# Kernel tuning notes

Hardware: AMD Instinct MI355X
Metric: run time of the kernel (lower is better)

Reference implementation:

```python
import jax, jax.numpy as jnp
import numpy as np

D_IN = 1024
D_OUT = 1024
N = 4096


def setup_inputs() -> dict:
    key = jax.random.key(0)
    ks = jax.random.split(key, 7)
    s_in = 1.0 / np.sqrt(D_IN)
    return {
        "x": jax.random.normal(ks[0], (N, D_IN), dtype=jnp.float32),
        "W_q": jax.random.uniform(ks[1], (D_IN, D_OUT), jnp.float32, -s_in, s_in),
        "b_q": jax.random.uniform(ks[2], (D_OUT,), jnp.float32, -s_in, s_in),
        "W_k": jax.random.uniform(ks[3], (D_IN, D_OUT), jnp.float32, -s_in, s_in),
        "b_k": jax.random.uniform(ks[4], (D_OUT,), jnp.float32, -s_in, s_in),
        "W_v": jax.random.uniform(ks[5], (D_IN, D_OUT), jnp.float32, -s_in, s_in),
        "b_v": jax.random.uniform(ks[6], (D_OUT,), jnp.float32, -s_in, s_in),
    }


def reference(x, W_q, b_q, W_k, b_k, W_v, b_v):
    # QKV projections (Linear with bias): [N, d_out]
    q = x @ W_q + b_q
    k = x @ W_k + b_k
    v = x @ W_v + b_v
    # Full attention: scores [N, N], scaled by sqrt(d_out)
    scores = (q @ k.T) / jnp.sqrt(jnp.asarray(k.shape[-1], q.dtype))
    attn = jax.nn.softmax(scores, axis=-1)
    return attn @ v  # [N, d_out]
```

## Files before the change

### kernel.cpp

```cpp
#include <hip/hip_runtime.h>

typedef __attribute__((ext_vector_type(8))) short short8;
typedef __attribute__((ext_vector_type(4))) float f32x4;
typedef __attribute__((ext_vector_type(8))) unsigned short ushort8;

typedef const unsigned int __attribute__((address_space(1)))* gas1_t;
typedef unsigned int __attribute__((address_space(3)))* las3_t;

__device__ __forceinline__ void gload_lds16(const void* g, void* l) {
  __builtin_amdgcn_global_load_lds((gas1_t)g, (las3_t)l, 16, 0, 0);
}

__device__ __forceinline__ unsigned short f2bf(float f) {
  unsigned int u = __float_as_uint(f);
  u += 0x7FFFu + ((u >> 16) & 1u);
  return (unsigned short)(u >> 16);
}
__device__ __forceinline__ float bf2f(unsigned short b) {
  return __uint_as_float(((unsigned int)b) << 16);
}

__global__ __launch_bounds__(256) void conv_f32_bf16(const float* __restrict__ in,
                                                     unsigned short* __restrict__ out, int n8) {
  int i = blockIdx.x * 256 + threadIdx.x;
  if (i >= n8) return;
  const f32x4* p = (const f32x4*)(in + (size_t)i * 8);
  f32x4 a = p[0], b = p[1];
  ushort8 o;
  o[0]=f2bf(a[0]); o[1]=f2bf(a[1]); o[2]=f2bf(a[2]); o[3]=f2bf(a[3]);
  o[4]=f2bf(b[0]); o[5]=f2bf(b[1]); o[6]=f2bf(b[2]); o[7]=f2bf(b[3]);
  *(ushort8*)(out + (size_t)i * 8) = o;
}

__global__ __launch_bounds__(256) void transconv_w(const float* __restrict__ Wq,
                                                   const float* __restrict__ Wk,
                                                   const float* __restrict__ Wv,
                                                   unsigned short* __restrict__ out) {
  __shared__ unsigned short tile[64][66];
  const float* W = (blockIdx.z == 0) ? Wq : ((blockIdx.z == 1) ? Wk : Wv);
  unsigned short* O = out + (size_t)blockIdx.z * 1048576;
  const int bi = blockIdx.x * 64;
  const int bo = blockIdx.y * 64;
#pragma unroll
  for (int p = 0; p < 16; ++p) {
    int idx = p * 256 + threadIdx.x;
    int r = idx >> 6, c = idx & 63;
    tile[r][c] = f2bf(W[(size_t)(bi + r) * 1024 + bo + c]);
  }
  __syncthreads();
#pragma unroll
  for (int p = 0; p < 16; ++p) {
    int idx = p * 256 + threadIdx.x;
    int r = idx >> 6, c = idx & 63;
    O[(size_t)(bo + r) * 1024 + bi + c] = tile[c][r];
  }
}

__global__ __launch_bounds__(256) void trans_bf16(const unsigned short* __restrict__ in,
                                                  unsigned short* __restrict__ out, int R, int C) {
  __shared__ unsigned short tile[64][66];
  const int br = blockIdx.x * 64, bc = blockIdx.y * 64;
#pragma unroll
  for (int p = 0; p < 16; ++p) {
    int idx = p * 256 + threadIdx.x;
    int r = idx >> 6, c = idx & 63;
    tile[r][c] = in[(size_t)(br + r) * C + bc + c];
  }
  __syncthreads();
#pragma unroll
  for (int p = 0; p < 16; ++p) {
    int idx = p * 256 + threadIdx.x;
    int r = idx >> 6, c = idx & 63;
    out[(size_t)(bc + r) * R + br + c] = tile[c][r];
  }
}

__global__ __launch_bounds__(256) void reduce_pv(const unsigned short* __restrict__ P,
                                                 const float* __restrict__ rsum,
                                                 float* __restrict__ out) {
  int i = blockIdx.x * 256 + threadIdx.x;
  const int m = (i * 8) >> 10;
  const float inv = 1.0f / rsum[m];
  float s[8] = {0.f, 0.f, 0.f, 0.f, 0.f, 0.f, 0.f, 0.f};
#pragma unroll
  for (int z = 0; z < 4; ++z) {
    ushort8 v = *(const ushort8*)(P + (size_t)z * 4194304 + (size_t)i * 8);
#pragma unroll
    for (int j = 0; j < 8; ++j) s[j] += bf2f(v[j]);
  }
  f32x4 o0, o1;
#pragma unroll
  for (int j = 0; j < 4; ++j) { o0[j] = s[j] * inv; o1[j] = s[4 + j] * inv; }
  f32x4* po = (f32x4*)(out + (size_t)i * 8);
  po[0] = o0; po[1] = o1;
}

template <int EPI>
__global__ __launch_bounds__(512, 1) void gemm256(
    const unsigned short* __restrict__ A, const unsigned short* __restrict__ B,
    int lda, int ldb, int K, void* __restrict__ C, int ldc,
    size_t strideBz, size_t strideCz,
    const float* __restrict__ bq, const float* __restrict__ bk, const float* __restrict__ bv,
    float scale, float* __restrict__ rsum) {
  __shared__ unsigned short As[2][2][8192];
  __shared__ unsigned short Bs[2][2][8192];
  const int tid = threadIdx.x;
  const int lane = tid & 63;
  const int w = tid >> 6;
  const int wr = w >> 2;
  const int wc = w & 3;
  const int l16 = lane & 15;
  const int q = lane >> 4;
  const int swq = (q ^ ((l16 >> 1) & 3)) * 8;

  const int nwgx = gridDim.x;
  const int nwg = nwgx * gridDim.y;
  const int lin = blockIdx.y * nwgx + blockIdx.x;
  const int swz = (lin & 7) * (nwg >> 3) + (lin >> 3);
  const int m0 = (swz / nwgx) * 256;
  const int n0 = (swz % nwgx) * 256;
  const int z = blockIdx.z;
  const unsigned short* Bz = B + (size_t)z * strideBz;
  const size_t koff = (EPI == 2) ? (size_t)z * K : 0;

  f32x4 acc[8][4];
#pragma unroll
  for (int i = 0; i < 8; ++i)
#pragma unroll
    for (int j = 0; j < 4; ++j) acc[i][j] = f32x4{0.f, 0.f, 0.f, 0.f};

  const unsigned short* apA[2][2];
  const unsigned short* apB[2][2];
#pragma unroll
  for (int ks = 0; ks < 2; ++ks)
#pragma unroll
    for (int j = 0; j < 2; ++j) {
      const int g = (j << 9) + tid;
      const int row = g >> 2;
      const int sq = (g & 3) ^ ((row >> 1) & 3);
      apA[ks][j] = A + (size_t)(m0 + row) * lda + koff + ks * 32 + sq * 8;
      apB[ks][j] = Bz + (size_t)(n0 + row) * ldb + koff + ks * 32 + sq * 8;
    }

#define STG_A(BUF, KS, K0)                                      \
  do {                                                          \
    gload_lds16(apA[KS][0] + (K0), &As[BUF][KS][tid * 8]);      \
    gload_lds16(apA[KS][1] + (K0), &As[BUF][KS][(512 + tid) * 8]); \
  } while (0)
#define STG_B(BUF, KS, K0)                                      \
  do {                                                          \
    gload_lds16(apB[KS][0] + (K0), &Bs[BUF][KS][tid * 8]);      \
    gload_lds16(apB[KS][1] + (K0), &Bs[BUF][KS][(512 + tid) * 8]); \
  } while (0)

  short8 bfr[4], afr[4];
#define LDB4(KS, BUF)                                                         \
  do {                                                                        \
    _Pragma("unroll") for (int _n = 0; _n < 4; ++_n) {                        \
      const int _r = wc * 64 + _n * 16 + l16;                                 \
      bfr[_n] = *(const short8*)(&Bs[BUF][KS][_r * 32 + swq]);                \
    }                                                                         \
  } while (0)
#define LDA4(KS, MH, BUF)                                                     \
  do {                                                                        \
    _Pragma("unroll") for (int _m = 0; _m < 4; ++_m) {                        \
      const int _r = wr * 128 + ((MH) * 4 + _m) * 16 + l16;                   \
      afr[_m] = *(const short8*)(&As[BUF][KS][_r * 32 + swq]);                \
    }                                                                         \
  } while (0)
#define MMP(MH)                                                               \
  do {                                                                        \
    __builtin_amdgcn_s_setprio(1);                                            \
    _Pragma("unroll") for (int _m = 0; _m < 4; ++_m)                          \
      _Pragma("unroll") for (int _n = 0; _n < 4; ++_n)                        \
        acc[(MH) * 4 + _m][_n] = __builtin_amdgcn_mfma_f32_16x16x32_bf16(     \
            afr[_m], bfr[_n], acc[(MH) * 4 + _m][_n], 0, 0, 0);               \
    __builtin_amdgcn_s_setprio(0);                                            \
  } while (0)
#define BAR asm volatile("s_barrier" ::: "memory")

  const int NT = K / 64;
  STG_B(0, 0, 0); STG_A(0, 0, 0); STG_B(0, 1, 0); STG_A(0, 1, 0);
  if (1 < NT) { STG_B(1, 0, 64); STG_A(1, 0, 64); STG_B(1, 1, 64); }
  if (1 < NT) asm volatile("s_waitcnt vmcnt(6)" ::: "memory");
  else        asm volatile("s_waitcnt vmcnt(0)" ::: "memory");
  BAR;

  for (int t = 0; t < NT; t += 2) {
    const bool more = (t + 2 < NT);
    const int k2 = (t + 2) * 64, k3 = (t + 3) * 64;
    LDB4(0, 0); LDA4(0, 0, 0);
    STG_A(1, 1, (t + 1) * 64);
    BAR; MMP(0); BAR;
    LDA4(0, 1, 0);
    if (more) STG_B(0, 0, k2);
    BAR; MMP(1); BAR;
    LDB4(1, 0); LDA4(1, 0, 0);
    if (more) STG_A(0, 0, k2);
    BAR; MMP(0); BAR;
    LDA4(1, 1, 0);
    if (more) STG_B(0, 1, k2);
    if (more) asm volatile("s_waitcnt vmcnt(6)" ::: "memory");
    else      asm volatile("s_waitcnt vmcnt(0)" ::: "memory");
    BAR; MMP(1); BAR;
    LDB4(0, 1); LDA4(0, 0, 1);
    if (more) STG_A(0, 1, k2);
    BAR; MMP(0); BAR;
    LDA4(0, 1, 1);
    if (more) STG_B(1, 0, k3);
    BAR; MMP(1); BAR;
    LDB4(1, 1); LDA4(1, 0, 1);
    if (more) STG_A(1, 0, k3);
    BAR; MMP(0); BAR;
    LDA4(1, 1, 1);
    if (more) {
      STG_B(1, 1, k3);
      asm volatile("s_waitcnt vmcnt(6)" ::: "memory");
    }
    BAR; MMP(1); BAR;
  }
#undef STG_A
#undef STG_B
#undef LDB4
#undef LDA4
#undef MMP
#undef BAR

  const int row0 = m0 + wr * 128 + q * 4;
  const int col0 = n0 + wc * 64;

  if constexpr (EPI == 0) {
    unsigned short* O = (unsigned short*)C + (size_t)z * strideCz;
    const float* bias = (z == 0) ? bq : ((z == 1) ? bk : bv);
#pragma unroll
    for (int mi = 0; mi < 8; ++mi)
#pragma unroll
      for (int ni = 0; ni < 4; ++ni) {
        const int col = col0 + ni * 16 + l16;
        const int row = row0 + mi * 16;
        float bvv = bias[col];
#pragma unroll
        for (int r = 0; r < 4; ++r)
          O[(size_t)(row + r) * ldc + col] = f2bf(acc[mi][ni][r] + bvv);
      }
  } else if constexpr (EPI == 1) {
    unsigned short* O = (unsigned short*)C;
#pragma unroll
    for (int mi = 0; mi < 8; ++mi) {
      float rs[4] = {0.f, 0.f, 0.f, 0.f};
      const int row = row0 + mi * 16;
#pragma unroll
      for (int ni = 0; ni < 4; ++ni) {
        const int col = col0 + ni * 16 + l16;
#pragma unroll
        for (int r = 0; r < 4; ++r) {
          unsigned short ub = f2bf(__expf(acc[mi][ni][r] * scale));
          O[(size_t)(row + r) * ldc + col] = ub;
          rs[r] += bf2f(ub);
        }
      }
#pragma unroll
      for (int off = 1; off <= 8; off <<= 1) {
#pragma unroll
        for (int r = 0; r < 4; ++r) rs[r] += __shfl_xor(rs[r], off);
      }
      if (l16 == 0) {
#pragma unroll
        for (int r = 0; r < 4; ++r) unsafeAtomicAdd(&rsum[row + r], rs[r]);
      }
    }
  } else {
    unsigned short* O = (unsigned short*)C + (size_t)z * strideCz;
#pragma unroll
    for (int mi = 0; mi < 8; ++mi)
#pragma unroll
      for (int ni = 0; ni < 4; ++ni) {
        const int col = col0 + ni * 16 + l16;
        const int row = row0 + mi * 16;
#pragma unroll
        for (int r = 0; r < 4; ++r)
          O[(size_t)(row + r) * ldc + col] = f2bf(acc[mi][ni][r]);
      }
  }
}

extern "C" void kernel_launch(void* const* d_in, const int* in_sizes, int n_in,
                              void* d_out, int out_size, void* d_ws, size_t ws_size,
                              hipStream_t stream) {
  const float* x  = (const float*)d_in[0];
  const float* Wq = (const float*)d_in[1];
  const float* bq = (const float*)d_in[2];
  const float* Wk = (const float*)d_in[3];
  const float* bk = (const float*)d_in[4];
  const float* Wv = (const float*)d_in[5];
  const float* bv = (const float*)d_in[6];
  float* out = (float*)d_out;
  char* ws = (char*)d_ws;
  const size_t MB = 1024 * 1024;

  unsigned short* xb  = (unsigned short*)(ws + 0);
  unsigned short* wt  = (unsigned short*)(ws + 8 * MB);
  unsigned short* qkv = (unsigned short*)(ws + 14 * MB);
  unsigned short* qb  = qkv;
  unsigned short* kb  = qkv + (size_t)4194304;
  unsigned short* vb  = qkv + (size_t)2 * 4194304;
  float*          rsum= (float*)(ws + 37 * MB);
  unsigned short* vt  = (unsigned short*)(ws + 38 * MB);
  unsigned short* S   = (unsigned short*)(ws + 46 * MB);
  unsigned short* P   = (unsigned short*)(ws + 0);

  conv_f32_bf16<<<2048, 256, 0, stream>>>(x, xb, 524288);
  transconv_w<<<dim3(16, 16, 3), 256, 0, stream>>>(Wq, Wk, Wv, wt);
  gemm256<0><<<dim3(4, 16, 3), 512, 0, stream>>>(
      xb, wt, 1024, 1024, 1024, qkv, 1024,
      (size_t)1048576, (size_t)4194304, bq, bk, bv, 1.0f, nullptr);
  trans_bf16<<<dim3(64, 16), 256, 0, stream>>>(vb, vt, 4096, 1024);
  hipMemsetAsync(rsum, 0, 4096 * sizeof(float), stream);
  gemm256<1><<<dim3(16, 16), 512, 0, stream>>>(
      qb, kb, 1024, 1024, 1024, S, 4096,
      (size_t)0, (size_t)0, nullptr, nullptr, nullptr, 0.03125f, rsum);
  gemm256<2><<<dim3(4, 16, 4), 512, 0, stream>>>(
      S, vt, 4096, 4096, 1024, P, 1024,
      (size_t)0, (size_t)4194304, nullptr, nullptr, nullptr, 1.0f, nullptr);
  reduce_pv<<<2048, 256, 0, stream>>>(P, rsum, out);
}
```

Baseline: 150.0 us.

## Replace direct global-to-LDS loads with register-staged prefetch pipeline in GEMM

```diff
diff --git a/kernel.cpp b/kernel.cpp
--- a/kernel.cpp
+++ b/kernel.cpp
@@ -3,13 +3,6 @@
 typedef __attribute__((ext_vector_type(8))) short short8;
 typedef __attribute__((ext_vector_type(4))) float f32x4;
 typedef __attribute__((ext_vector_type(8))) unsigned short ushort8;
-
-typedef const unsigned int __attribute__((address_space(1)))* gas1_t;
-typedef unsigned int __attribute__((address_space(3)))* las3_t;
-
-__device__ __forceinline__ void gload_lds16(const void* g, void* l) {
-  __builtin_amdgcn_global_load_lds((gas1_t)g, (las3_t)l, 16, 0, 0);
-}
 
 __device__ __forceinline__ unsigned short f2bf(float f) {
   unsigned int u = __float_as_uint(f);
@@ -142,16 +135,16 @@
       apB[ks][j] = Bz + (size_t)(n0 + row) * ldb + koff + ks * 32 + sq * 8;
     }
 
-#define STG_A(BUF, KS, K0)                                      \
-  do {                                                          \
-    gload_lds16(apA[KS][0] + (K0), &As[BUF][KS][tid * 8]);      \
-    gload_lds16(apA[KS][1] + (K0), &As[BUF][KS][(512 + tid) * 8]); \
-  } while (0)
-#define STG_B(BUF, KS, K0)                                      \
-  do {                                                          \
-    gload_lds16(apB[KS][0] + (K0), &Bs[BUF][KS][tid * 8]);      \
-    gload_lds16(apB[KS][1] + (K0), &Bs[BUF][KS][(512 + tid) * 8]); \
-  } while (0)
+  ushort8 r0a, r0b, r1a, r1b, r2a, r2b, r3a, r3b;
+
+#define ISS_A(RS, KS, K0) do { RS##a = *(const ushort8*)(apA[KS][0] + (K0)); \
+                               RS##b = *(const ushort8*)(apA[KS][1] + (K0)); } while (0)
+#define ISS_B(RS, KS, K0) do { RS##a = *(const ushort8*)(apB[KS][0] + (K0)); \
+                               RS##b = *(const ushort8*)(apB[KS][1] + (K0)); } while (0)
+#define WRT_A(RS, BUF, KS) do { *(ushort8*)(&As[BUF][KS][tid * 8]) = RS##a; \
+                                *(ushort8*)(&As[BUF][KS][(512 + tid) * 8]) = RS##b; } while (0)
+#define WRT_B(RS, BUF, KS) do { *(ushort8*)(&Bs[BUF][KS][tid * 8]) = RS##a; \
+                                *(ushort8*)(&Bs[BUF][KS][(512 + tid) * 8]) = RS##b; } while (0)
 
   short8 bfr[4], afr[4];
 #define LDB4(KS, BUF)                                                         \
@@ -177,53 +170,61 @@
             afr[_m], bfr[_n], acc[(MH) * 4 + _m][_n], 0, 0, 0);               \
     __builtin_amdgcn_s_setprio(0);                                            \
   } while (0)
+#define FLUSH asm volatile("s_waitcnt lgkmcnt(0)" ::: "memory")
 #define BAR asm volatile("s_barrier" ::: "memory")
 
   const int NT = K / 64;
-  STG_B(0, 0, 0); STG_A(0, 0, 0); STG_B(0, 1, 0); STG_A(0, 1, 0);
-  if (1 < NT) { STG_B(1, 0, 64); STG_A(1, 0, 64); STG_B(1, 1, 64); }
-  if (1 < NT) asm volatile("s_waitcnt vmcnt(6)" ::: "memory");
-  else        asm volatile("s_waitcnt vmcnt(0)" ::: "memory");
-  BAR;
+  ISS_B(r0, 0, 0); ISS_A(r1, 0, 0); ISS_B(r2, 1, 0); ISS_A(r3, 1, 0);
+  WRT_B(r0, 0, 0); WRT_A(r1, 0, 0); WRT_B(r2, 0, 1); WRT_A(r3, 0, 1);
+  ISS_B(r0, 0, 64); ISS_A(r1, 0, 64); ISS_B(r2, 1, 64);
+  WRT_B(r0, 1, 0); WRT_A(r1, 1, 0); WRT_B(r2, 1, 1);
+  ISS_A(r0, 1, 64);
+  ISS_B(r1, 0, 128);
+  ISS_A(r2, 0, 128);
+  ISS_B(r3, 1, 128);
+  FLUSH; BAR;
 
   for (int t = 0; t < NT; t += 2) {
-    const bool more = (t + 2 < NT);
-    const int k2 = (t + 2) * 64, k3 = (t + 3) * 64;
+    const bool more  = (t + 2 < NT);
+    const bool more2 = (t + 4 < NT);
+    const int k2 = (t + 2) * 64, k3 = (t + 3) * 64, k4 = (t + 4) * 64;
     LDB4(0, 0); LDA4(0, 0, 0);
-    STG_A(1, 1, (t + 1) * 64);
-    BAR; MMP(0); BAR;
+    WRT_A(r0, 1, 1);
+    if (more) ISS_A(r0, 1, k2);
+    FLUSH; BAR; MMP(0); BAR;
     LDA4(0, 1, 0);
-    if (more) STG_B(0, 0, k2);
-    BAR; MMP(1); BAR;
+    if (more) { WRT_B(r1, 0, 0); ISS_B(r1, 0, k3); }
+    FLUSH; BAR; MMP(1); BAR;
     LDB4(1, 0); LDA4(1, 0, 0);
-    if (more) STG_A(0, 0, k2);
-    BAR; MMP(0); BAR;
+    if (more) { WRT_A(r2, 0, 0); ISS_A(r2, 0, k3); }
+    FLUSH; BAR; MMP(0); BAR;
     LDA4(1, 1, 0);
-    if (more) STG_B(0, 1, k2);
-    if (more) asm volatile("s_waitcnt vmcnt(6)" ::: "memory");
-    else      asm volatile("s_waitcnt vmcnt(0)" ::: "memory");
-    BAR; MMP(1); BAR;
+    if (more) { WRT_B(r3, 0, 1); ISS_B(r3, 1, k3); }
+    FLUSH; BAR; MMP(1); BAR;
     LDB4(0, 1); LDA4(0, 0, 1);
-    if (more) STG_A(0, 1, k2);
-    BAR; MMP(0); BAR;
+    if (more) { WRT_A(r0, 0, 1); ISS_A(r0, 1, k3); }
+    FLUSH; BAR; MMP(0); BAR;
     LDA4(0, 1, 1);
-    if (more) STG_B(1, 0, k3);
-    BAR; MMP(1); BAR;
+    if (more) WRT_B(r1, 1, 0);
+    if (more2) ISS_B(r1, 0, k4);
+    FLUSH; BAR; MMP(1); BAR;
     LDB4(1, 1); LDA4(1, 0, 1);
-    if (more) STG_A(1, 0, k3);
-    BAR; MMP(0); BAR;
+    if (more) WRT_A(r2, 1, 0);
+    if (more2) ISS_A(r2, 0, k4);
+    FLUSH; BAR; MMP(0); BAR;
     LDA4(1, 1, 1);
-    if (more) {
-      STG_B(1, 1, k3);
-      asm volatile("s_waitcnt vmcnt(6)" ::: "memory");
-    }
-    BAR; MMP(1); BAR;
-  }
-#undef STG_A
-#undef STG_B
+    if (more) WRT_B(r3, 1, 1);
+    if (more2) ISS_B(r3, 1, k4);
+    FLUSH; BAR; MMP(1); BAR;
+  }
+#undef ISS_A
+#undef ISS_B
+#undef WRT_A
+#undef WRT_B
 #undef LDB4
 #undef LDA4
 #undef MMP
+#undef FLUSH
 #undef BAR
 
   const int row0 = m0 + wr * 128 + q * 4;
```

Result: slower. 198.6 us (+32.4%).
